# Kernel optimization log

Hardware: AMD Instinct MI355X
Metric: run time of the kernel (lower is better)

The kernel has to match this reference:

```python
import jax, jax.numpy as jnp
import numpy as np
from math import sqrt

N = 8192      # points
I = 16        # in_channels
H = 64        # hidden_units
O = 64        # out_channels
CUTS = 8      # conv MLP intermediate width
RADIUS = 9.0
GROUPS = 4    # GroupNorm groups
BLK = 128     # i-block size for tiled pairwise reduction (KeOps-style)


def _leaky(x):
    return jnp.where(x >= 0, x, 0.2 * x)


def _group_norm(f, w, b, eps=1e-5):
    # torch GroupNorm applied to (1, C, N): stats per group over (C//G channels x N points)
    n, c = f.shape
    g = f.reshape(n, GROUPS, c // GROUPS)
    m = g.mean(axis=(0, 2), keepdims=True)
    v = ((g - m) ** 2).mean(axis=(0, 2), keepdims=True)
    g = (g - m) * jax.lax.rsqrt(v + eps)
    return g.reshape(n, c) * w + b


def setup_inputs() -> dict:
    key = jax.random.key(0)
    ks = jax.random.split(key, 20)
    U = lambda k, s, lim: jax.random.uniform(k, s, minval=-lim, maxval=lim)
    points = jax.random.normal(ks[0], (N, 3), dtype=jnp.float32)
    nuv = jax.random.normal(ks[1], (N, 3, 3), dtype=jnp.float32)
    features = jax.random.normal(ks[2], (N, I), dtype=jnp.float32)
    # net_in (torch Linear default init)
    W_in1 = U(ks[3], (H, I), 1 / np.sqrt(I)); b_in1 = U(ks[4], (H,), 1 / np.sqrt(I))
    W_in2 = U(ks[5], (H, H), 1 / np.sqrt(H)); b_in2 = U(ks[6], (H,), 1 / np.sqrt(H))
    # conv MLP with custom init from the module
    A1 = jax.random.normal(ks[7], (CUTS, 3), dtype=jnp.float32)
    B1 = jax.random.uniform(ks[8], (CUTS,)) * 0.8 * jnp.sqrt((A1 ** 2).sum(-1))
    A2 = U(ks[9], (H, CUTS), 1 / np.sqrt(CUTS))
    B2 = jax.random.normal(ks[10], (H,)) * 0.5 * jnp.sqrt((A2 ** 2).sum(-1))
    # net_out
    W_out1 = U(ks[11], (O, H), 1 / np.sqrt(H)); b_out1 = U(ks[12], (O,), 1 / np.sqrt(H))
    W_out2 = U(ks[13], (O, O), 1 / np.sqrt(O)); b_out2 = U(ks[14], (O,), 1 / np.sqrt(O))
    return {
        "points": points, "nuv": nuv, "features": features,
        "W_in1": W_in1, "b_in1": b_in1, "W_in2": W_in2, "b_in2": b_in2,
        "gn_in_w": jnp.ones((H,), jnp.float32), "gn_in_b": jnp.zeros((H,), jnp.float32),
        "A1": A1, "B1": B1, "A2": A2, "B2": B2,
        "W_out1": W_out1, "b_out1": b_out1, "W_out2": W_out2, "b_out2": b_out2,
        "gn_out_w": jnp.ones((O,), jnp.float32), "gn_out_b": jnp.zeros((O,), jnp.float32),
    }


def _forward(points, nuv, features, W_in1, b_in1, W_in2, b_in2, gn_in_w, gn_in_b,
             A1, B1, A2, B2, W_out1, b_out1, W_out2, b_out2, gn_out_w, gn_out_b):
    # 1. net_in + GroupNorm
    f = _leaky(features @ W_in1.T + b_in1)
    f = _leaky(f @ W_in2.T + b_in2)
    f = _group_norm(f, gn_in_w, gn_in_b)          # (N, H)
    # 2. quasi-geodesic interaction, tiled over i-blocks (KeOps-style)
    pts = points / (sqrt(2.0) * RADIUS)
    normals = jax.lax.stop_gradient(nuv[:, 0, :])  # n_j is detached in the original
    nblk = N // BLK

    def body(carry, blk):
        xi, nuvi = blk                              # (B,3), (B,3,3)
        ni = nuvi[:, 0, :]                          # (B,3) n_i (not detached)
        diff = pts[None, :, :] - xi[:, None, :]     # (B,N,3) x_j - x_i
        dn = ni @ normals.T                         # (B,N) <n_i, n_j>
        d2 = (diff ** 2).sum(-1) * (2.0 - dn) ** 2  # pseudo-geodesic squared dist
        w = jnp.exp(-d2)                            # Gaussian window
        X = jnp.einsum('bij,bnj->bni', nuvi, diff)  # coords in local basis (B,N,3)
        h = jax.nn.relu(jnp.einsum('bnj,cj->bnc', X, A1) + B1)   # (B,N,CUTS)
        g = jax.nn.relu(jnp.einsum('bnc,hc->bnh', h, A2) + B2)   # (B,N,H)
        out = jnp.einsum('bn,bnh,nh->bh', w, g, f)  # sum_j w_ij * conv(P_ij) * f_j
        return carry, out

    _, outs = jax.lax.scan(
        body, None, (pts.reshape(nblk, BLK, 3), nuv.reshape(nblk, BLK, 3, 3)))
    f2 = outs.reshape(N, H)
    # 3. net_out + GroupNorm
    f2 = _leaky(f2 @ W_out1.T + b_out1)
    f2 = _leaky(f2 @ W_out2.T + b_out2)
    f2 = _group_norm(f2, gn_out_w, gn_out_b)       # (N, O)
    return f2


def reference(points, nuv, features, W_in1, b_in1, W_in2, b_in2, gn_in_w, gn_in_b,
              A1, B1, A2, B2, W_out1, b_out1, W_out2, b_out2, gn_out_w, gn_out_b):
    return _forward(points, nuv, features, W_in1, b_in1, W_in2, b_in2, gn_in_w, gn_in_b,
                    A1, B1, A2, B2, W_out1, b_out1, W_out2, b_out2, gn_out_w, gn_out_b)
```

## Files before the change

kernel.cpp:

```cpp
#include <hip/hip_runtime.h>
#include <hip/hip_bf16.h>
#include <stdint.h>


#define N_PTS   8192
#define CHUNK   64
#define NCHUNK  (N_PTS / CHUNK)
#define WPB     8
#define PSCALE  0.07856742013183861f
#define GN_CNT  (N_PTS * 16)

#define OFF_POINTS 0
#define OFF_NUV    24576
#define OFF_FEAT   98304
#define OFF_WIN1   229376
#define OFF_BIN1   230400
#define OFF_WIN2   230464
#define OFF_BIN2   234560
#define OFF_GNIW   234624
#define OFF_GNIB   234688
#define OFF_A1     234752
#define OFF_B1     234776
#define OFF_A2     234784
#define OFF_B2     235296
#define OFF_WOUT1  235360
#define OFF_BOUT1  239456
#define OFF_WOUT2  239520
#define OFF_BOUT2  243616
#define OFF_GNOW   243680
#define OFF_GNOB   243744
#define CVT_TOTAL  243808
#define NSEG 19

typedef _Float16 half2_t __attribute__((ext_vector_type(2)));
typedef _Float16 f16x8   __attribute__((ext_vector_type(8)));
typedef float    f32x2   __attribute__((ext_vector_type(2)));
typedef float    f32x4   __attribute__((ext_vector_type(4)));

struct InPtrs { const void* p[NSEG]; };

__device__ __forceinline__ float rfl(float x) {
  return __int_as_float(__builtin_amdgcn_readfirstlane(__float_as_int(x)));
}
__device__ __forceinline__ float leaky(float x) { return x > 0.f ? x : 0.2f * x; }

#if __has_builtin(__builtin_amdgcn_cvt_pkrtz)
__device__ __forceinline__ half2_t pk16(float a, float b) {
  return __builtin_bit_cast(half2_t, __builtin_amdgcn_cvt_pkrtz(a, b));
}
#else
__device__ __forceinline__ half2_t pk16(float a, float b) {
  half2_t r; r.x = (_Float16)a; r.y = (_Float16)b; return r;
}
#endif

__global__ __launch_bounds__(256) void prep_kernel(InPtrs ptrs, float* dst,
                                                   float* gstats) {
  if (blockIdx.x == 0 && threadIdx.x < 16) gstats[threadIdx.x] = 0.f;
  const uint32_t w0 = ((const uint32_t*)ptrs.p[7])[0];
  const bool bf = (w0 != 0x3F800000u);
  const int CUM[NSEG + 1] = {0, 24576, 98304, 229376, 230400, 230464, 234560,
                             234624, 234688, 234752, 234776, 234784, 235296,
                             235360, 239456, 239520, 243616, 243680, 243744,
                             243808};
  for (int e = blockIdx.x * 256 + threadIdx.x; e < CVT_TOTAL;
       e += gridDim.x * 256) {
    int s = 0;
#pragma unroll
    for (int i = 1; i < NSEG; ++i) s += (e >= CUM[i]) ? 1 : 0;
    const int rem = e - CUM[s];
    float v = bf ? __bfloat162float(((const __hip_bfloat16*)ptrs.p[s])[rem])
                 : ((const float*)ptrs.p[s])[rem];
    if (s == 0) v *= PSCALE;
    dst[e] = v;
  }
}

__global__ __launch_bounds__(256) void pack_kernel(
    const float* __restrict__ pool, float4* __restrict__ ppk,
    float4* __restrict__ npk) {
  const int n = blockIdx.x * 256 + threadIdx.x;
  const float px = pool[OFF_POINTS + n * 3 + 0];
  const float py = pool[OFF_POINTS + n * 3 + 1];
  const float pz = pool[OFF_POINTS + n * 3 + 2];
  float4 p; p.x = px; p.y = py; p.z = pz;
  p.w = fmaf(px, px, fmaf(py, py, pz * pz));
  ppk[n] = p;
  float4 q;
  q.x = pool[OFF_NUV + n * 9 + 0];
  q.y = pool[OFF_NUV + n * 9 + 1];
  q.z = pool[OFF_NUV + n * 9 + 2];
  q.w = 0.f;
  npk[n] = q;
}

__global__ __launch_bounds__(256) void mlp_in_kernel(
    const float* __restrict__ pool, float* __restrict__ fbuf) {
  __shared__ float ls[4][64];
  const int t = threadIdx.x, nl = t >> 6, h = t & 63;
  const int n = blockIdx.x * 4 + nl;
  const float4* fr = (const float4*)(pool + OFF_FEAT + n * 16);
  const float4* w1 = (const float4*)(pool + OFF_WIN1 + h * 16);
  float a = pool[OFF_BIN1 + h];
#pragma unroll
  for (int k = 0; k < 4; ++k) {
    const float4 x = fr[k], w = w1[k];
    a = fmaf(x.x, w.x, a); a = fmaf(x.y, w.y, a);
    a = fmaf(x.z, w.z, a); a = fmaf(x.w, w.w, a);
  }
  ls[nl][h] = leaky(a);
  __syncthreads();
  const float4* w2 = (const float4*)(pool + OFF_WIN2 + h * 64);
  const float4* lr = (const float4*)&ls[nl][0];
  float c = pool[OFF_BIN2 + h];
#pragma unroll
  for (int k = 0; k < 16; ++k) {
    const float4 x = lr[k], w = w2[k];
    c = fmaf(x.x, w.x, c); c = fmaf(x.y, w.y, c);
    c = fmaf(x.z, w.z, c); c = fmaf(x.w, w.w, c);
  }
  fbuf[n * 64 + h] = leaky(c);
}

__global__ __launch_bounds__(256) void mlp_out_kernel(
    const float* __restrict__ cbuf, const float* __restrict__ pool,
    float* __restrict__ obuf) {
  __shared__ float ls[4][64];
  const int t = threadIdx.x, nl = t >> 6, h = t & 63;
  const int n = blockIdx.x * 4 + nl;
  const float4* cr = (const float4*)(cbuf + n * 64);
  const float4* w1 = (const float4*)(pool + OFF_WOUT1 + h * 64);
  float a = pool[OFF_BOUT1 + h];
#pragma unroll
  for (int k = 0; k < 16; ++k) {
    const float4 x = cr[k], w = w1[k];
    a = fmaf(x.x, w.x, a); a = fmaf(x.y, w.y, a);
    a = fmaf(x.z, w.z, a); a = fmaf(x.w, w.w, a);
  }
  ls[nl][h] = leaky(a);
  __syncthreads();
  const float4* w2 = (const float4*)(pool + OFF_WOUT2 + h * 64);
  const float4* lr = (const float4*)&ls[nl][0];
  float c = pool[OFF_BOUT2 + h];
#pragma unroll
  for (int k = 0; k < 16; ++k) {
    const float4 x = lr[k], w = w2[k];
    c = fmaf(x.x, w.x, c); c = fmaf(x.y, w.y, c);
    c = fmaf(x.z, w.z, c); c = fmaf(x.w, w.w, c);
  }
  obuf[n * 64 + h] = leaky(c);
}

__global__ __launch_bounds__(256) void gn_stats_kernel(
    const float* __restrict__ buf, float* __restrict__ gstats) {
  __shared__ float red[8];
  const int t = threadIdx.x;
  const int g = (t & 63) >> 4;
  if (t < 8) red[t] = 0.f;
  float s = 0.f, q = 0.f;
  for (int idx = blockIdx.x * 256 + t; idx < N_PTS * 64; idx += 64 * 256) {
    const float v = buf[idx];
    s += v; q = fmaf(v, v, q);
  }
  __syncthreads();
  atomicAdd(&red[g], s);
  atomicAdd(&red[4 + g], q);
  __syncthreads();
  if (t < 8) atomicAdd(&gstats[t], red[t]);
}

__global__ __launch_bounds__(256) void gn_apply_Q_kernel(
    const float* __restrict__ buf, const float* __restrict__ gstats,
    const float* __restrict__ pool, float4* __restrict__ bufq) {
  __shared__ float tile[64][68];
  const int t = threadIdx.x;
  const int c = blockIdx.x;
  const int n0 = c * 64;
  const int rr = t >> 4;
  const int cc4 = (t & 15) * 4;
  const int g = cc4 >> 4;
  const float m = gstats[g] * (1.f / GN_CNT);
  const float v = gstats[4 + g] * (1.f / GN_CNT) - m * m;
  const float rs = rsqrtf(fmaxf(v, 0.f) + 1e-5f);
  const float4 gw = *(const float4*)&pool[OFF_GNIW + cc4];
  const float4 gb = *(const float4*)&pool[OFF_GNIB + cc4];
#pragma unroll
  for (int r = 0; r < 4; ++r) {
    const int row = rr + 16 * r;
    const float4 x = *(const float4*)&buf[(n0 + row) * 64 + cc4];
    float4 o;
    o.x = fmaf((x.x - m) * rs, gw.x, gb.x);
    o.y = fmaf((x.y - m) * rs, gw.y, gb.y);
    o.z = fmaf((x.z - m) * rs, gw.z, gb.z);
    o.w = fmaf((x.w - m) * rs, gw.w, gb.w);
    *(float4*)&tile[row][cc4] = o;
  }
  __syncthreads();
#pragma unroll
  for (int si = 0; si < 4; ++si) {
    const int s = t + 256 * si;
    const int region = s >> 6, lane = s & 63;
    const int jt = region >> 2, ht = region & 3;
    const int kg = lane >> 4, l15 = lane & 15;
    const int jb = 16 * jt + 4 * kg, h = 16 * ht + l15;
    float4 o;
    o.x = tile[jb + 0][h];
    o.y = tile[jb + 1][h];
    o.z = tile[jb + 2][h];
    o.w = tile[jb + 3][h];
    bufq[c * 1024 + s] = o;
  }
}

__global__ __launch_bounds__(256) void gn_apply_out_kernel(
    const float* __restrict__ buf, const float* __restrict__ gstats,
    const float* __restrict__ pool, void* __restrict__ out,
    const uint32_t* __restrict__ dref) {
  const bool bf = (dref[0] != 0x3F800000u);
  const int idx = blockIdx.x * 256 + threadIdx.x;
  const int h = idx & 63, g = h >> 4;
  const float m = gstats[g] * (1.f / GN_CNT);
  const float v = gstats[4 + g] * (1.f / GN_CNT) - m * m;
  const float rs = rsqrtf(fmaxf(v, 0.f) + 1e-5f);
  const float r = fmaf((buf[idx] - m) * rs, pool[OFF_GNOW + h], pool[OFF_GNOB + h]);
  if (bf) ((__hip_bfloat16*)out)[idx] = __float2bfloat16(r);
  else    ((float*)out)[idx] = r;
}

__global__ __launch_bounds__(512) void conv_kernel(
    const float* __restrict__ pool, const float4* __restrict__ fq,
    float* __restrict__ cbuf, const float4* __restrict__ ppk,
    const float4* __restrict__ npk) {
  __shared__ float4 f_q[1024];
  __shared__ float4 hcA[WPB][4][32];
  __shared__ float4 zero4_s;

  const int t = threadIdx.x;
  const int wv = t >> 6, lane = t & 63;
  const int b = blockIdx.x * WPB + wv;
  const int kg  = lane >> 4;
  const int l15 = lane & 15;

  const float pbx = rfl(pool[OFF_POINTS + b * 3 + 0]);
  const float pby = rfl(pool[OFF_POINTS + b * 3 + 1]);
  const float pbz = rfl(pool[OFF_POINTS + b * 3 + 2]);
  float nb[9];
#pragma unroll
  for (int i = 0; i < 9; ++i) nb[i] = rfl(pool[OFF_NUV + b * 9 + i]);
  const float pbsq = rfl(fmaf(pbx, pbx, fmaf(pby, pby, pbz * pbz)));

  float mM[24], mc[8];
#pragma unroll
  for (int cc = 0; cc < 8; ++cc) {
    const float a0 = pool[OFF_A1 + cc * 3 + 0];
    const float a1 = pool[OFF_A1 + cc * 3 + 1];
    const float a2 = pool[OFF_A1 + cc * 3 + 2];
#pragma unroll
    for (int j = 0; j < 3; ++j)
      mM[cc * 3 + j] =
          rfl(fmaf(a0, nb[j], fmaf(a1, nb[3 + j], a2 * nb[6 + j])));
    mc[cc] = rfl(fmaf(-mM[cc * 3 + 0], pbx,
                 fmaf(-mM[cc * 3 + 1], pby,
                 fmaf(-mM[cc * 3 + 2], pbz, pool[OFF_B1 + cc]))));
  }

  f16x8 bfrag[4];
#pragma unroll
  for (int ht = 0; ht < 4; ++ht) {
    const int h = 16 * ht + l15;
#pragma unroll
    for (int i = 0; i < 8; ++i) {
      float v = 0.f;
      if (kg == 0) v = pool[OFF_A2 + h * 8 + i];
      else if (kg == 1 && i == 0) v = pool[OFF_B2 + h];
      bfrag[ht][i] = (_Float16)v;
    }
  }

  {
    float4 z4; z4.x = 0.f; z4.y = 0.f; z4.z = 0.f; z4.w = 0.f;
    if (lane < 32) {
#pragma unroll
      for (int jt = 0; jt < 4; ++jt) hcA[wv][jt][lane] = z4;
    }
    if (t == 0) zero4_s = z4;
  }

  const f32x4 kzero = {0.f, 0.f, 0.f, 0.f};
  f32x2 acc01[4], acc23[4];
#pragma unroll
  for (int ht = 0; ht < 4; ++ht) {
    acc01[ht].x = 0.f; acc01[ht].y = 0.f;
    acc23[ht].x = 0.f; acc23[ht].y = 0.f;
  }

  for (int c = 0; c < NCHUNK; ++c) {
    const float4 fv0 = fq[c * 1024 + t];
    const float4 fv1 = fq[c * 1024 + t + 512];
    const float4 pv = ppk[c * CHUNK + lane];
    const float4 nv = npk[c * CHUNK + lane];

    __syncthreads();
    f_q[t]       = fv0;
    f_q[t + 512] = fv1;

    const float dotp = fmaf(pv.x, pbx, fmaf(pv.y, pby, pv.z * pbz));
    const float dd   = fmaf(-2.f, dotp, pv.w + pbsq);
    const float dn   = fmaf(nb[0], nv.x, fmaf(nb[1], nv.y, nb[2] * nv.z));
    const float ttv  = 2.f - dn;
    const float wexp = __expf(-dd * ttv * ttv);
    float hc[8];
#pragma unroll
    for (int cc = 0; cc < 8; ++cc)
      hc[cc] = wexp * fmaxf(fmaf(mM[cc * 3 + 0], pv.x,
                            fmaf(mM[cc * 3 + 1], pv.y,
                            fmaf(mM[cc * 3 + 2], pv.z, mc[cc]))), 0.f);
    float4 lo;
    lo.x = __builtin_bit_cast(float, pk16(hc[0], hc[1]));
    lo.y = __builtin_bit_cast(float, pk16(hc[2], hc[3]));
    lo.z = __builtin_bit_cast(float, pk16(hc[4], hc[5]));
    lo.w = __builtin_bit_cast(float, pk16(hc[6], hc[7]));
    hcA[wv][lane >> 4][l15] = lo;
    ((float*)&hcA[wv][lane >> 4][16 + l15])[0] =
        __builtin_bit_cast(float, pk16(wexp, 0.f));

    __syncthreads();

#pragma unroll
    for (int jt = 0; jt < 4; ++jt) {
      const float4* ap = (kg < 2) ? &hcA[wv][jt][kg * 16 + l15] : &zero4_s;
      const f16x8 af = __builtin_bit_cast(f16x8, *ap);
#pragma unroll
      for (int ht = 0; ht < 4; ++ht) {
        const f32x4 D = __builtin_amdgcn_mfma_f32_16x16x32_f16(
            af, bfrag[ht], kzero, 0, 0, 0);
        const float4 fv = f_q[(jt * 4 + ht) * 64 + lane];
        f32x2 fq01, fq23, q01, q23;
        fq01.x = fv.x; fq01.y = fv.y;
        fq23.x = fv.z; fq23.y = fv.w;
        q01.x = fmaxf(D[0], 0.f); q01.y = fmaxf(D[1], 0.f);
        q23.x = fmaxf(D[2], 0.f); q23.y = fmaxf(D[3], 0.f);
        asm("v_pk_fma_f32 %0, %1, %2, %0"
            : "+v"(acc01[ht]) : "v"(fq01), "v"(q01));
        asm("v_pk_fma_f32 %0, %1, %2, %0"
            : "+v"(acc23[ht]) : "v"(fq23), "v"(q23));
      }
    }
  }

  float accf[4];
#pragma unroll
  for (int ht = 0; ht < 4; ++ht) {
    float a = (acc01[ht].x + acc01[ht].y) + (acc23[ht].x + acc23[ht].y);
    a += __shfl_xor(a, 16, 64);
    a += __shfl_xor(a, 32, 64);
    accf[ht] = a;
  }
  if (lane < 16) {
#pragma unroll
    for (int ht = 0; ht < 4; ++ht)
      cbuf[b * 64 + 16 * ht + lane] = accf[ht];
  }
}

extern "C" void kernel_launch(void* const* d_in, const int* in_sizes, int n_in,
                              void* d_out, int out_size, void* d_ws, size_t ws_size,
                              hipStream_t stream) {
  (void)in_sizes; (void)n_in; (void)out_size; (void)ws_size;
  const uint32_t* dref = (const uint32_t*)d_in[7];

  float* pool   = (float*)d_ws;
  float* fbuf   = pool + CVT_TOTAL;
  float* cbuf   = fbuf + N_PTS * 64;
  float* gstats = cbuf + N_PTS * 64;
  float* fbufq  = gstats + 16;
  float* ppk    = fbufq + N_PTS * 64;
  float* npk    = ppk + N_PTS * 4;

  InPtrs ptrs;
  for (int i = 0; i < NSEG; ++i) ptrs.p[i] = d_in[i];

  prep_kernel<<<256, 256, 0, stream>>>(ptrs, pool, gstats);
  pack_kernel<<<N_PTS / 256, 256, 0, stream>>>(pool, (float4*)ppk, (float4*)npk);
  mlp_in_kernel<<<N_PTS / 4, 256, 0, stream>>>(pool, fbuf);
  gn_stats_kernel<<<64, 256, 0, stream>>>(fbuf, gstats);
  gn_apply_Q_kernel<<<NCHUNK, 256, 0, stream>>>(fbuf, gstats, pool,
                                                (float4*)fbufq);
  conv_kernel<<<N_PTS / WPB, 512, 0, stream>>>(pool, (const float4*)fbufq,
                                               cbuf, (const float4*)ppk,
                                               (const float4*)npk);
  mlp_out_kernel<<<N_PTS / 4, 256, 0, stream>>>(cbuf, pool, fbuf);
  gn_stats_kernel<<<64, 256, 0, stream>>>(fbuf, gstats + 8);
  gn_apply_out_kernel<<<N_PTS * 64 / 256, 256, 0, stream>>>(
      fbuf, gstats + 8, pool, d_out, dref);
}
```

Measured before the change: 697.9 us.

## Process two query points per wavefront in conv kernel to reuse staged tiles

Each wavefront now handles two query points instead of one, so each block covers 16 points and the grid is halved. The per-chunk global loads of features, packed points and normals, the LDS staging and the barriers are shared across both queries, and each LDS feature read feeds two MFMAs and two sets of FMAs. The cost is roughly double the per-query registers (transform matrices and accumulators) plus a doubled hcA shared buffer, which can lower occupancy. Only the first query's values go through the uniform-register hint.

```diff
diff --git a/kernel.cpp b/kernel.cpp
--- a/kernel.cpp
+++ b/kernel.cpp
@@ -7,6 +7,7 @@
 #define CHUNK   64
 #define NCHUNK  (N_PTS / CHUNK)
 #define WPB     8
+#define QPB     16
 #define PSCALE  0.07856742013183861f
 #define GN_CNT  (N_PTS * 16)
 
@@ -232,36 +233,48 @@
     float* __restrict__ cbuf, const float4* __restrict__ ppk,
     const float4* __restrict__ npk) {
   __shared__ float4 f_q[1024];
-  __shared__ float4 hcA[WPB][4][32];
+  __shared__ float4 hcA[2][WPB][4][32];
   __shared__ float4 zero4_s;
 
   const int t = threadIdx.x;
   const int wv = t >> 6, lane = t & 63;
-  const int b = blockIdx.x * WPB + wv;
+  const int bb = blockIdx.x * QPB + wv;
   const int kg  = lane >> 4;
   const int l15 = lane & 15;
 
-  const float pbx = rfl(pool[OFF_POINTS + b * 3 + 0]);
-  const float pby = rfl(pool[OFF_POINTS + b * 3 + 1]);
-  const float pbz = rfl(pool[OFF_POINTS + b * 3 + 2]);
-  float nb[9];
-#pragma unroll
-  for (int i = 0; i < 9; ++i) nb[i] = rfl(pool[OFF_NUV + b * 9 + i]);
-  const float pbsq = rfl(fmaf(pbx, pbx, fmaf(pby, pby, pbz * pbz)));
-
-  float mM[24], mc[8];
-#pragma unroll
-  for (int cc = 0; cc < 8; ++cc) {
-    const float a0 = pool[OFF_A1 + cc * 3 + 0];
-    const float a1 = pool[OFF_A1 + cc * 3 + 1];
-    const float a2 = pool[OFF_A1 + cc * 3 + 2];
-#pragma unroll
-    for (int j = 0; j < 3; ++j)
-      mM[cc * 3 + j] =
-          rfl(fmaf(a0, nb[j], fmaf(a1, nb[3 + j], a2 * nb[6 + j])));
-    mc[cc] = rfl(fmaf(-mM[cc * 3 + 0], pbx,
-                 fmaf(-mM[cc * 3 + 1], pby,
-                 fmaf(-mM[cc * 3 + 2], pbz, pool[OFF_B1 + cc]))));
+  float mMq[2][24], mcq[2][8];
+  float pbxq[2], pbyq[2], pbzq[2], pbsq[2], n0q[2][3];
+#pragma unroll
+  for (int q = 0; q < 2; ++q) {
+    const int b = bb + 8 * q;
+    float px = pool[OFF_POINTS + b * 3 + 0];
+    float py = pool[OFF_POINTS + b * 3 + 1];
+    float pz = pool[OFF_POINTS + b * 3 + 2];
+    float nbl[9];
+#pragma unroll
+    for (int i = 0; i < 9; ++i) nbl[i] = pool[OFF_NUV + b * 9 + i];
+    if (q == 0) {
+      px = rfl(px); py = rfl(py); pz = rfl(pz);
+#pragma unroll
+      for (int i = 0; i < 9; ++i) nbl[i] = rfl(nbl[i]);
+    }
+    pbxq[q] = px; pbyq[q] = py; pbzq[q] = pz;
+    pbsq[q] = fmaf(px, px, fmaf(py, py, pz * pz));
+    n0q[q][0] = nbl[0]; n0q[q][1] = nbl[1]; n0q[q][2] = nbl[2];
+#pragma unroll
+    for (int cc = 0; cc < 8; ++cc) {
+      const float a0 = rfl(pool[OFF_A1 + cc * 3 + 0]);
+      const float a1 = rfl(pool[OFF_A1 + cc * 3 + 1]);
+      const float a2 = rfl(pool[OFF_A1 + cc * 3 + 2]);
+#pragma unroll
+      for (int j = 0; j < 3; ++j)
+        mMq[q][cc * 3 + j] =
+            fmaf(a0, nbl[j], fmaf(a1, nbl[3 + j], a2 * nbl[6 + j]));
+      mcq[q][cc] = fmaf(-mMq[q][cc * 3 + 0], px,
+                   fmaf(-mMq[q][cc * 3 + 1], py,
+                   fmaf(-mMq[q][cc * 3 + 2], pz,
+                        rfl(pool[OFF_B1 + cc]))));
+    }
   }
 
   f16x8 bfrag[4];
@@ -281,18 +294,22 @@
     float4 z4; z4.x = 0.f; z4.y = 0.f; z4.z = 0.f; z4.w = 0.f;
     if (lane < 32) {
 #pragma unroll
-      for (int jt = 0; jt < 4; ++jt) hcA[wv][jt][lane] = z4;
+      for (int q = 0; q < 2; ++q)
+#pragma unroll
+        for (int jt = 0; jt < 4; ++jt) hcA[q][wv][jt][lane] = z4;
     }
     if (t == 0) zero4_s = z4;
   }
 
   const f32x4 kzero = {0.f, 0.f, 0.f, 0.f};
-  f32x2 acc01[4], acc23[4];
-#pragma unroll
-  for (int ht = 0; ht < 4; ++ht) {
-    acc01[ht].x = 0.f; acc01[ht].y = 0.f;
-    acc23[ht].x = 0.f; acc23[ht].y = 0.f;
-  }
+  f32x2 acc01[2][4], acc23[2][4];
+#pragma unroll
+  for (int q = 0; q < 2; ++q)
+#pragma unroll
+    for (int ht = 0; ht < 4; ++ht) {
+      acc01[q][ht].x = 0.f; acc01[q][ht].y = 0.f;
+      acc23[q][ht].x = 0.f; acc23[q][ht].y = 0.f;
+    }
 
   for (int c = 0; c < NCHUNK; ++c) {
     const float4 fv0 = fq[c * 1024 + t];
@@ -304,62 +321,83 @@
     f_q[t]       = fv0;
     f_q[t + 512] = fv1;
 
-    const float dotp = fmaf(pv.x, pbx, fmaf(pv.y, pby, pv.z * pbz));
-    const float dd   = fmaf(-2.f, dotp, pv.w + pbsq);
-    const float dn   = fmaf(nb[0], nv.x, fmaf(nb[1], nv.y, nb[2] * nv.z));
-    const float ttv  = 2.f - dn;
-    const float wexp = __expf(-dd * ttv * ttv);
-    float hc[8];
-#pragma unroll
-    for (int cc = 0; cc < 8; ++cc)
-      hc[cc] = wexp * fmaxf(fmaf(mM[cc * 3 + 0], pv.x,
-                            fmaf(mM[cc * 3 + 1], pv.y,
-                            fmaf(mM[cc * 3 + 2], pv.z, mc[cc]))), 0.f);
-    float4 lo;
-    lo.x = __builtin_bit_cast(float, pk16(hc[0], hc[1]));
-    lo.y = __builtin_bit_cast(float, pk16(hc[2], hc[3]));
-    lo.z = __builtin_bit_cast(float, pk16(hc[4], hc[5]));
-    lo.w = __builtin_bit_cast(float, pk16(hc[6], hc[7]));
-    hcA[wv][lane >> 4][l15] = lo;
-    ((float*)&hcA[wv][lane >> 4][16 + l15])[0] =
-        __builtin_bit_cast(float, pk16(wexp, 0.f));
+#pragma unroll
+    for (int q = 0; q < 2; ++q) {
+      const float dotp = fmaf(pv.x, pbxq[q], fmaf(pv.y, pbyq[q],
+                              pv.z * pbzq[q]));
+      const float dd   = fmaf(-2.f, dotp, pv.w + pbsq[q]);
+      const float dn   = fmaf(n0q[q][0], nv.x, fmaf(n0q[q][1], nv.y,
+                              n0q[q][2] * nv.z));
+      const float ttv  = 2.f - dn;
+      const float wexp = __expf(-dd * ttv * ttv);
+      float hc[8];
+#pragma unroll
+      for (int cc = 0; cc < 8; ++cc)
+        hc[cc] = wexp * fmaxf(fmaf(mMq[q][cc * 3 + 0], pv.x,
+                              fmaf(mMq[q][cc * 3 + 1], pv.y,
+                              fmaf(mMq[q][cc * 3 + 2], pv.z,
+                                   mcq[q][cc]))), 0.f);
+      float4 lo;
+      lo.x = __builtin_bit_cast(float, pk16(hc[0], hc[1]));
+      lo.y = __builtin_bit_cast(float, pk16(hc[2], hc[3]));
+      lo.z = __builtin_bit_cast(float, pk16(hc[4], hc[5]));
+      lo.w = __builtin_bit_cast(float, pk16(hc[6], hc[7]));
+      hcA[q][wv][lane >> 4][l15] = lo;
+      ((float*)&hcA[q][wv][lane >> 4][16 + l15])[0] =
+          __builtin_bit_cast(float, pk16(wexp, 0.f));
+    }
 
     __syncthreads();
 
 #pragma unroll
     for (int jt = 0; jt < 4; ++jt) {
-      const float4* ap = (kg < 2) ? &hcA[wv][jt][kg * 16 + l15] : &zero4_s;
-      const f16x8 af = __builtin_bit_cast(f16x8, *ap);
+      const float4* apA = (kg < 2) ? &hcA[0][wv][jt][kg * 16 + l15] : &zero4_s;
+      const float4* apB = (kg < 2) ? &hcA[1][wv][jt][kg * 16 + l15] : &zero4_s;
+      const f16x8 afA = __builtin_bit_cast(f16x8, *apA);
+      const f16x8 afB = __builtin_bit_cast(f16x8, *apB);
 #pragma unroll
       for (int ht = 0; ht < 4; ++ht) {
-        const f32x4 D = __builtin_amdgcn_mfma_f32_16x16x32_f16(
-            af, bfrag[ht], kzero, 0, 0, 0);
         const float4 fv = f_q[(jt * 4 + ht) * 64 + lane];
-        f32x2 fq01, fq23, q01, q23;
+        f32x2 fq01, fq23;
         fq01.x = fv.x; fq01.y = fv.y;
         fq23.x = fv.z; fq23.y = fv.w;
-        q01.x = fmaxf(D[0], 0.f); q01.y = fmaxf(D[1], 0.f);
-        q23.x = fmaxf(D[2], 0.f); q23.y = fmaxf(D[3], 0.f);
+        const f32x4 DA = __builtin_amdgcn_mfma_f32_16x16x32_f16(
+            afA, bfrag[ht], kzero, 0, 0, 0);
+        const f32x4 DB = __builtin_amdgcn_mfma_f32_16x16x32_f16(
+            afB, bfrag[ht], kzero, 0, 0, 0);
+        f32x2 qa01, qa23, qb01, qb23;
+        qa01.x = fmaxf(DA[0], 0.f); qa01.y = fmaxf(DA[1], 0.f);
+        qa23.x = fmaxf(DA[2], 0.f); qa23.y = fmaxf(DA[3], 0.f);
+        qb01.x = fmaxf(DB[0], 0.f); qb01.y = fmaxf(DB[1], 0.f);
+        qb23.x = fmaxf(DB[2], 0.f); qb23.y = fmaxf(DB[3], 0.f);
         asm("v_pk_fma_f32 %0, %1, %2, %0"
-            : "+v"(acc01[ht]) : "v"(fq01), "v"(q01));
+            : "+v"(acc01[0][ht]) : "v"(fq01), "v"(qa01));
         asm("v_pk_fma_f32 %0, %1, %2, %0"
-            : "+v"(acc23[ht]) : "v"(fq23), "v"(q23));
+            : "+v"(acc23[0][ht]) : "v"(fq23), "v"(qa23));
+        asm("v_pk_fma_f32 %0, %1, %2, %0"
+            : "+v"(acc01[1][ht]) : "v"(fq01), "v"(qb01));
+        asm("v_pk_fma_f32 %0, %1, %2, %0"
+            : "+v"(acc23[1][ht]) : "v"(fq23), "v"(qb23));
       }
     }
   }
 
-  float accf[4];
-#pragma unroll
-  for (int ht = 0; ht < 4; ++ht) {
-    float a = (acc01[ht].x + acc01[ht].y) + (acc23[ht].x + acc23[ht].y);
-    a += __shfl_xor(a, 16, 64);
-    a += __shfl_xor(a, 32, 64);
-    accf[ht] = a;
-  }
-  if (lane < 16) {
-#pragma unroll
-    for (int ht = 0; ht < 4; ++ht)
-      cbuf[b * 64 + 16 * ht + lane] = accf[ht];
+#pragma unroll
+  for (int q = 0; q < 2; ++q) {
+    float accf[4];
+#pragma unroll
+    for (int ht = 0; ht < 4; ++ht) {
+      float a = (acc01[q][ht].x + acc01[q][ht].y) +
+                (acc23[q][ht].x + acc23[q][ht].y);
+      a += __shfl_xor(a, 16, 64);
+      a += __shfl_xor(a, 32, 64);
+      accf[ht] = a;
+    }
+    if (lane < 16) {
+#pragma unroll
+      for (int ht = 0; ht < 4; ++ht)
+        cbuf[(bb + 8 * q) * 64 + 16 * ht + lane] = accf[ht];
+    }
   }
 }
 
@@ -386,7 +424,7 @@
   gn_stats_kernel<<<64, 256, 0, stream>>>(fbuf, gstats);
   gn_apply_Q_kernel<<<NCHUNK, 256, 0, stream>>>(fbuf, gstats, pool,
                                                 (float4*)fbufq);
-  conv_kernel<<<N_PTS / WPB, 512, 0, stream>>>(pool, (const float4*)fbufq,
+  conv_kernel<<<N_PTS / QPB, 512, 0, stream>>>(pool, (const float4*)fbufq,
                                                cbuf, (const float4*)ppk,
                                                (const float4*)npk);
   mlp_out_kernel<<<N_PTS / 4, 256, 0, stream>>>(cbuf, pool, fbuf);
```

Result: slower. 760.2 us (+8.9%).
